# Optimization experiments

Hardware: AMD Instinct MI355X
Metric: run time of the kernel (lower is better)

## Reference

```python
import jax, jax.numpy as jnp
import numpy as np

N_NODES = 50000
N_EDGES = 800000
IN_C, HID_C, OUT_C = 128, 256, 64


def _linear_params(key, fan_in, fan_out):
    kw, kb = jax.random.split(key)
    bound = 1.0 / np.sqrt(fan_in)
    w = jax.random.uniform(kw, (fan_in, fan_out), jnp.float32, -bound, bound)
    b = jax.random.uniform(kb, (fan_out,), jnp.float32, -bound, bound)
    return w, b


def setup_inputs() -> dict:
    key = jax.random.key(0)
    ks = jax.random.split(key, 8)
    x = jax.random.normal(ks[0], (N_NODES, IN_C), jnp.float32)
    edge_index = jax.random.randint(ks[1], (2, N_EDGES), 0, N_NODES, dtype=jnp.int64)
    w1a, b1a = _linear_params(ks[2], IN_C, HID_C)
    w1b, b1b = _linear_params(ks[3], HID_C, HID_C)
    w2a, b2a = _linear_params(ks[4], HID_C, HID_C)
    w2b, b2b = _linear_params(ks[5], HID_C, HID_C)
    w3a, b3a = _linear_params(ks[6], HID_C, HID_C)
    w3b, b3b = _linear_params(ks[7], HID_C, OUT_C)
    return {
        "x": x, "edge_index": edge_index,
        "w1a": w1a, "b1a": b1a, "w1b": w1b, "b1b": b1b,
        "w2a": w2a, "b2a": b2a, "w2b": w2b, "b2b": b2b,
        "w3a": w3a, "b3a": b3a, "w3b": w3b, "b3b": b3b,
    }


def _gin_conv(x, src, dst, wa, ba, wb, bb):
    # GINConv (eps=0): MLP( x + sum_{j->i} x_j )
    agg = jax.ops.segment_sum(x[src], dst, num_segments=N_NODES)  # [N, d]
    h = x + agg
    h = jnp.maximum(h @ wa + ba, 0.0)
    return h @ wb + bb


def reference(x, edge_index, w1a, b1a, w1b, b1b, w2a, b2a, w2b, b2b,
              w3a, b3a, w3b, b3b):
    src, dst = edge_index[0], edge_index[1]
    h = jnp.maximum(_gin_conv(x, src, dst, w1a, b1a, w1b, b1b), 0.0)
    h = jnp.maximum(_gin_conv(h, src, dst, w2a, b2a, w2b, b2b), 0.0)
    # output head: Linear -> ReLU -> Dropout(eval: identity) -> Linear
    h = jnp.maximum(h @ w3a + b3a, 0.0)
    return h @ w3b + b3b  # [N, OUT_C]
```

## Files before the change

kernel.cpp:

```cpp
#include <hip/hip_runtime.h>
#include <stdint.h>

#define N_NODES 50000
#define N_EDGES 800000
#define M_PAD   50048
#define NREP    4
#define MCAP    8
#define SCAP    24
#define CSTR    50048
#define TSTR    264

typedef __attribute__((ext_vector_type(8))) short bf16x8;
typedef __attribute__((ext_vector_type(4))) float f32x4;

__device__ __forceinline__ unsigned short f2b(float f){
    unsigned int u = __builtin_bit_cast(unsigned int, f);
    u += 0x7fffu + ((u >> 16) & 1u);
    return (unsigned short)(u >> 16);
}
__device__ __forceinline__ float b2f(unsigned short s){
    unsigned int u = ((unsigned int)s) << 16;
    return __builtin_bit_cast(float, u);
}

__device__ __forceinline__ void gl_lds16(const void* g, void* l){
    __builtin_amdgcn_global_load_lds(
        (const __attribute__((address_space(1))) void*)g,
        (__attribute__((address_space(3))) void*)l, 16, 0, 0);
}

__global__ void k_x2b(const float* __restrict__ x, unsigned short* __restrict__ xs,
                      int* __restrict__ cnt){
    int gi = blockIdx.x * 256 + threadIdx.x;
    if (gi < NREP * CSTR) cnt[gi] = 0;
    size_t e0 = (size_t)gi * 8;
    if (e0 >= (size_t)M_PAD * 128) return;
    int node = (int)(e0 >> 7);
    int ch0  = (int)(e0 & 127);
    int sl = ch0 >> 5, wth = ch0 & 31;
    bf16x8 o;
    if (node < N_NODES){
        const float4* xp = (const float4*)(x + e0);
        float4 a = xp[0], b = xp[1];
        o[0] = (short)f2b(a.x); o[1] = (short)f2b(a.y);
        o[2] = (short)f2b(a.z); o[3] = (short)f2b(a.w);
        o[4] = (short)f2b(b.x); o[5] = (short)f2b(b.y);
        o[6] = (short)f2b(b.z); o[7] = (short)f2b(b.w);
    } else {
#pragma unroll
        for (int i = 0; i < 8; ++i) o[i] = 0;
    }
    *(bf16x8*)&xs[((size_t)(sl * 50048 + node)) * 32 + wth] = o;
}

__global__ void k_scatter(const int* __restrict__ ei, int* __restrict__ cnt,
                          unsigned short* __restrict__ mn, unsigned short* __restrict__ sp){
    int e = blockIdx.x * 256 + threadIdx.x;
    if (e < N_EDGES){
        unsigned d = (unsigned)ei[N_EDGES + e];
        unsigned s = (unsigned)ei[e];
        if (d < N_NODES && s < N_NODES){
            int r = threadIdx.x & 3;
            int p = atomicAdd(&cnt[r * CSTR + d], 1);
            int b = (d << 2) + r;
            if (p < MCAP) mn[(b << 3) + p] = (unsigned short)s;
            else if (p < MCAP + SCAP) sp[b * SCAP + (p - MCAP)] = (unsigned short)s;
        }
    }
}

template<int C, bool SPLIT>
__global__ __launch_bounds__(256) void k_aggx(const unsigned short* __restrict__ in,
        const int* __restrict__ cnt, const unsigned short* __restrict__ mn,
        const unsigned short* __restrict__ sp, unsigned short* __restrict__ out){
    constexpr int RS = C / 8;
    const int bid = blockIdx.x, w8 = bid & 7;
    int g, nbase;
    if (SPLIT){ g = w8 & 3; nbase = ((bid >> 3) + (w8 >> 2) * 1564) * 16; }
    else      { g = w8;     nbase = (bid >> 3) * 16; }
    const int lane = threadIdx.x & 63, wid = threadIdx.x >> 6;
    const int qd = lane >> 2, lq = lane & 3;
    const int nl = qd >> 2, r = qd & 3;
    const int n = nbase + wid * 4 + nl;
    const bf16x8* xr = (const bf16x8*)in;
    const size_t sb = (size_t)g * 50048;
    const int jz = N_NODES;

    float a[8];
#pragma unroll
    for (int i = 0; i < 8; ++i) a[i] = 0.f;

    int c = cnt[r * CSTR + n];
    int cr = (c > MCAP + SCAP) ? (MCAP + SCAP) : c;
    int c8 = (cr > MCAP) ? MCAP : cr;
    const unsigned short* mb = &mn[((n << 2) + r) << 3];
    ushort4 u0 = *(const ushort4*)mb;
    ushort4 u1 = *(const ushort4*)(mb + 4);

    {
        int j0 = (c8 > 0) ? (int)u0.x : jz;
        int j1 = (c8 > 1) ? (int)u0.y : jz;
        int j2 = (c8 > 2) ? (int)u0.z : jz;
        int j3 = (c8 > 3) ? (int)u0.w : jz;
        bf16x8 v0 = xr[(sb + j0) * 4 + lq];
        bf16x8 v1 = xr[(sb + j1) * 4 + lq];
        bf16x8 v2 = xr[(sb + j2) * 4 + lq];
        bf16x8 v3 = xr[(sb + j3) * 4 + lq];
#pragma unroll
        for (int i = 0; i < 8; ++i)
            a[i] += (b2f((unsigned short)v0[i]) + b2f((unsigned short)v1[i]))
                  + (b2f((unsigned short)v2[i]) + b2f((unsigned short)v3[i]));
    }
    if (c8 > 4){
        int j4 = (int)u1.x;
        int j5 = (c8 > 5) ? (int)u1.y : jz;
        int j6 = (c8 > 6) ? (int)u1.z : jz;
        int j7 = (c8 > 7) ? (int)u1.w : jz;
        bf16x8 v0 = xr[(sb + j4) * 4 + lq];
        bf16x8 v1 = xr[(sb + j5) * 4 + lq];
        bf16x8 v2 = xr[(sb + j6) * 4 + lq];
        bf16x8 v3 = xr[(sb + j7) * 4 + lq];
#pragma unroll
        for (int i = 0; i < 8; ++i)
            a[i] += (b2f((unsigned short)v0[i]) + b2f((unsigned short)v1[i]))
                  + (b2f((unsigned short)v2[i]) + b2f((unsigned short)v3[i]));
    }
    if (cr > MCAP){
        const unsigned short* sb2 = &sp[((n << 2) + r) * SCAP];
        for (int k = MCAP; k < cr; ++k){
            int j = sb2[k - MCAP];
            bf16x8 v = xr[(sb + j) * 4 + lq];
#pragma unroll
            for (int i = 0; i < 8; ++i) a[i] += b2f((unsigned short)v[i]);
        }
    }
#pragma unroll
    for (int i = 0; i < 8; ++i){
        a[i] += __shfl_xor(a[i], 4);
        a[i] += __shfl_xor(a[i], 8);
    }
    if (r == 0){
        bf16x8 o;
        if (n < N_NODES){
            bf16x8 s = xr[(sb + n) * 4 + lq];
#pragma unroll
            for (int i = 0; i < 8; ++i) o[i] = (short)f2b(a[i] + b2f((unsigned short)s[i]));
        } else {
#pragma unroll
            for (int i = 0; i < 8; ++i) o[i] = 0;
        }
        *(bf16x8*)&out[((size_t)n * RS + g * 4 + lq) * 8] = o;
    }
}

__global__ void k_wt_all(const float* w0, const float* w1, const float* w2,
                         const float* w3, const float* w4, const float* w5,
                         unsigned short* o0, unsigned short* o1, unsigned short* o2,
                         unsigned short* o3, unsigned short* o4, unsigned short* o5){
    const int Ks[6]  = {128, 256, 256, 256, 256, 256};
    const int Ns[6]  = {256, 256, 256, 256, 256,  64};
    const int NPs[6] = {256, 256, 256, 256, 256, 128};
    int s = blockIdx.y;
    const float* w = (s == 0) ? w0 : (s == 1) ? w1 : (s == 2) ? w2
                   : (s == 3) ? w3 : (s == 4) ? w4 : w5;
    unsigned short* o = (s == 0) ? o0 : (s == 1) ? o1 : (s == 2) ? o2
                      : (s == 3) ? o3 : (s == 4) ? o4 : o5;
    int K = Ks[s], N = Ns[s], NP = NPs[s];
    int idx = blockIdx.x * 256 + threadIdx.x;
    if (idx >= NP * K) return;
    int np = idx / K, k = idx - np * K;
    float v = (np < N) ? w[(size_t)k * N + np] : 0.f;
    o[idx] = f2b(v);
}

template<int K1, int NMID, int NOUT, bool RELU_OUT, bool BF16OUT, bool SLICED>
__global__ __launch_bounds__(256) void k_mlp2(const unsigned short* __restrict__ A,
        const unsigned short* __restrict__ WA, const float* __restrict__ bA,
        const unsigned short* __restrict__ WB, const float* __restrict__ bB,
        void* __restrict__ out, int mstore){
    constexpr int NFA = NMID / 32;
    constexpr int NFB = NOUT / 32;
    __shared__ alignas(16) unsigned short As[64 * 32];
    __shared__ alignas(16) unsigned short Bs[NMID * 32];
    __shared__ alignas(16) unsigned short T[64 * TSTR];
    const int tid  = threadIdx.x;
    const int lane = tid & 63;
    const int c = lane & 15, qq = lane >> 4;
    const int kk = qq * 8;
    const int row0 = blockIdx.x * 64;
    const int wm = (tid >> 6) >> 1, wn = (tid >> 6) & 1;

    const f32x4 fzero = {0.f, 0.f, 0.f, 0.f};
    const char* Ab = (const char*)A;

    {
        f32x4 acc[NFA][2];
#pragma unroll
        for (int nf = 0; nf < NFA; ++nf){ acc[nf][0] = fzero; acc[nf][1] = fzero; }
        const char* Wb = (const char*)WA;
        for (int kt = 0; kt < K1 / 32; ++kt){
            {
                const int o = tid * 16;
                gl_lds16(Ab + ((size_t)(row0 + (o >> 6)) * K1 + kt * 32) * 2 + (o & 63),
                         (char*)As + o);
            }
#pragma unroll
            for (int ch = 0; ch < NMID / 64; ++ch){
                const int o = ch * 4096 + tid * 16;
                gl_lds16(Wb + ((size_t)(o >> 6) * K1 + kt * 32) * 2 + (o & 63),
                         (char*)Bs + o);
            }
            __syncthreads();
            bf16x8 xf[2];
#pragma unroll
            for (int mf = 0; mf < 2; ++mf)
                xf[mf] = *(const bf16x8*)&As[(wm * 32 + mf * 16 + c) * 32 + kk];
#pragma unroll
            for (int nf = 0; nf < NFA; ++nf){
                bf16x8 wf = *(const bf16x8*)&Bs[((wn * NFA + nf) * 16 + c) * 32 + kk];
#pragma unroll
                for (int mf = 0; mf < 2; ++mf)
                    acc[nf][mf] = __builtin_amdgcn_mfma_f32_16x16x32_bf16(wf, xf[mf], acc[nf][mf], 0, 0, 0);
            }
            __syncthreads();
        }
#pragma unroll
        for (int nf = 0; nf < NFA; ++nf){
            const int nb = wn * (NFA * 16) + nf * 16 + qq * 4;
            const float4 bb = *(const float4*)&bA[nb];
#pragma unroll
            for (int mf = 0; mf < 2; ++mf){
                const int ml = wm * 32 + mf * 16 + c;
                float v0 = fmaxf(acc[nf][mf][0] + bb.x, 0.f);
                float v1 = fmaxf(acc[nf][mf][1] + bb.y, 0.f);
                float v2 = fmaxf(acc[nf][mf][2] + bb.z, 0.f);
                float v3 = fmaxf(acc[nf][mf][3] + bb.w, 0.f);
                uint2 p;
                p.x = (unsigned)f2b(v0) | ((unsigned)f2b(v1) << 16);
                p.y = (unsigned)f2b(v2) | ((unsigned)f2b(v3) << 16);
                *(uint2*)&T[ml * TSTR + nb] = p;
            }
        }
    }
    __syncthreads();

    {
        f32x4 acc[NFB][2];
#pragma unroll
        for (int nf = 0; nf < NFB; ++nf){ acc[nf][0] = fzero; acc[nf][1] = fzero; }
        const char* Wb = (const char*)WB;
        for (int kt = 0; kt < NMID / 32; ++kt){
#pragma unroll
            for (int ch = 0; ch < NOUT / 64; ++ch){
                const int o = ch * 4096 + tid * 16;
                gl_lds16(Wb + ((size_t)(o >> 6) * NMID + kt * 32) * 2 + (o & 63),
                         (char*)Bs + o);
            }
            __syncthreads();
            bf16x8 xf[2];
#pragma unroll
            for (int mf = 0; mf < 2; ++mf)
                xf[mf] = *(const bf16x8*)&T[(wm * 32 + mf * 16 + c) * TSTR + kt * 32 + kk];
#pragma unroll
            for (int nf = 0; nf < NFB; ++nf){
                bf16x8 wf = *(const bf16x8*)&Bs[((wn * NFB + nf) * 16 + c) * 32 + kk];
#pragma unroll
                for (int mf = 0; mf < 2; ++mf)
                    acc[nf][mf] = __builtin_amdgcn_mfma_f32_16x16x32_bf16(wf, xf[mf], acc[nf][mf], 0, 0, 0);
            }
            __syncthreads();
        }
#pragma unroll
        for (int nf = 0; nf < NFB; ++nf){
            const int nb = wn * (NFB * 16) + nf * 16 + qq * 4;
            const float4 bb = *(const float4*)&bB[nb];
#pragma unroll
            for (int mf = 0; mf < 2; ++mf){
                const int m = row0 + wm * 32 + mf * 16 + c;
                if (m < mstore){
                    float v0 = acc[nf][mf][0] + bb.x;
                    float v1 = acc[nf][mf][1] + bb.y;
                    float v2 = acc[nf][mf][2] + bb.z;
                    float v3 = acc[nf][mf][3] + bb.w;
                    if (RELU_OUT){
                        v0 = fmaxf(v0, 0.f); v1 = fmaxf(v1, 0.f);
                        v2 = fmaxf(v2, 0.f); v3 = fmaxf(v3, 0.f);
                    }
                    if (SLICED){
                        uint2 p;
                        p.x = (unsigned)f2b(v0) | ((unsigned)f2b(v1) << 16);
                        p.y = (unsigned)f2b(v2) | ((unsigned)f2b(v3) << 16);
                        if (m >= N_NODES){ p.x = 0; p.y = 0; }
                        *(uint2*)&((unsigned short*)out)[
                            ((size_t)((nb >> 5) * 50048 + m)) * 32 + (nb & 31)] = p;
                    } else if (BF16OUT){
                        uint2 p;
                        p.x = (unsigned)f2b(v0) | ((unsigned)f2b(v1) << 16);
                        p.y = (unsigned)f2b(v2) | ((unsigned)f2b(v3) << 16);
                        *(uint2*)&((unsigned short*)out)[(size_t)m * NOUT + nb] = p;
                    } else {
                        float4 p = make_float4(v0, v1, v2, v3);
                        *(float4*)&((float*)out)[(size_t)m * NOUT + nb] = p;
                    }
                }
            }
        }
    }
}

extern "C" void kernel_launch(void* const* d_in, const int* in_sizes, int n_in,
                              void* d_out, int out_size, void* d_ws, size_t ws_size,
                              hipStream_t stream){
    const float* x   = (const float*)d_in[0];
    const int*   ei  = (const int*)d_in[1];
    const float* w1a = (const float*)d_in[2];
    const float* b1a = (const float*)d_in[3];
    const float* w1b = (const float*)d_in[4];
    const float* b1b = (const float*)d_in[5];
    const float* w2a = (const float*)d_in[6];
    const float* b2a = (const float*)d_in[7];
    const float* w2b = (const float*)d_in[8];
    const float* b2b = (const float*)d_in[9];
    const float* w3a = (const float*)d_in[10];
    const float* b3a = (const float*)d_in[11];
    const float* w3b = (const float*)d_in[12];
    const float* b3b = (const float*)d_in[13];

    char* ws = (char*)d_ws;
    size_t off = 0;
    auto take = [&](size_t bytes) -> char* {
        off = (off + 255) & ~(size_t)255;
        char* p = ws + off;
        off += bytes;
        return p;
    };
    unsigned short* xs1  = (unsigned short*)take((size_t)4 * 50048 * 32 * 2);
    unsigned short* g1   = (unsigned short*)take((size_t)M_PAD * 128 * 2);
    unsigned short* h1s  = (unsigned short*)take((size_t)8 * 50048 * 32 * 2);
    unsigned short* g2   = (unsigned short*)take((size_t)M_PAD * 256 * 2);
    unsigned short* h2   = (unsigned short*)take((size_t)M_PAD * 256 * 2);
    unsigned short* wt1a = (unsigned short*)take(256 * 128 * 2);
    unsigned short* wt1b = (unsigned short*)take(256 * 256 * 2);
    unsigned short* wt2a = (unsigned short*)take(256 * 256 * 2);
    unsigned short* wt2b = (unsigned short*)take(256 * 256 * 2);
    unsigned short* wt3a = (unsigned short*)take(256 * 256 * 2);
    unsigned short* wt3b = (unsigned short*)take(128 * 256 * 2);
    int*            cnt  = (int*)take((size_t)NREP * CSTR * 4);
    unsigned short* mn   = (unsigned short*)take((size_t)M_PAD * 4 * MCAP * 2);
    unsigned short* sp   = (unsigned short*)take((size_t)M_PAD * 4 * SCAP * 2);

    k_x2b<<<(M_PAD * 128 / 8 + 255) / 256, 256, 0, stream>>>(x, xs1, cnt);
    k_scatter<<<(N_EDGES + 255) / 256, 256, 0, stream>>>(ei, cnt, mn, sp);
    k_wt_all<<<dim3(256, 6), 256, 0, stream>>>(w1a, w1b, w2a, w2b, w3a, w3b,
                                               wt1a, wt1b, wt2a, wt2b, wt3a, wt3b);

    k_aggx<128, true ><<<1564 * 8, 256, 0, stream>>>(xs1, cnt, mn, sp, g1);
    k_mlp2<128, 256, 256, true, true, true><<<M_PAD / 64, 256, 0, stream>>>(
        g1, wt1a, b1a, wt1b, b1b, h1s, M_PAD);
    k_aggx<256, false><<<3128 * 8, 256, 0, stream>>>(h1s, cnt, mn, sp, g2);
    k_mlp2<256, 256, 256, true, true, false><<<M_PAD / 64, 256, 0, stream>>>(
        g2, wt2a, b2a, wt2b, b2b, h2, M_PAD);
    k_mlp2<256, 256, 64, false, false, false><<<M_PAD / 64, 256, 0, stream>>>(
        h2, wt3a, b3a, wt3b, b3b, d_out, N_NODES);
}
```

Measured before the change: 235.2 us.

## Merge replicated neighbor buckets into per-node padded lists before aggregation

Adds a merge kernel that compacts the four replicated per-node neighbor buckets (main plus spill) into one contiguous list per node, padded to a multiple of four with a sentinel index. The aggregation kernel then assigns one quad of lanes per node instead of four quads, loops over groups of four gathers, and drops the cross-replica shuffle reduction and the conditional spill loop. This targets lane waste and divergence from uneven bucket fill, at the cost of an extra kernel and buffer. Lists are capped at 64 neighbors per node.

```diff
diff --git a/kernel.cpp b/kernel.cpp
--- a/kernel.cpp
+++ b/kernel.cpp
@@ -8,6 +8,7 @@
 #define MCAP    8
 #define SCAP    24
 #define CSTR    50048
+#define LCAP    64
 #define TSTR    264
 
 typedef __attribute__((ext_vector_type(8))) short bf16x8;
@@ -69,88 +70,80 @@
     }
 }
 
+__global__ void k_merge(const int* __restrict__ cnt, const unsigned short* __restrict__ mn,
+                        const unsigned short* __restrict__ sp,
+                        unsigned short* __restrict__ mg, int* __restrict__ gcnt){
+    const int t = threadIdx.x;
+    const int r = t & 3;
+    const int n = blockIdx.x * 64 + (t >> 2);
+    int c = cnt[r * CSTR + n];
+    if (c > MCAP + SCAP) c = MCAP + SCAP;
+    int incl = c;
+    int t1 = __shfl_up(incl, 1, 4); if (r >= 1) incl += t1;
+    int t2 = __shfl_up(incl, 2, 4); if (r >= 2) incl += t2;
+    const int excl = incl - c;
+    const int total = __shfl(incl, 3, 4);
+    const unsigned mb = (unsigned)n * LCAP;
+    const unsigned short* src = &mn[((n << 2) + r) << 3];
+    for (int i = 0; i < c && i < MCAP; ++i){
+        int pos = excl + i;
+        if (pos < LCAP) mg[mb + pos] = src[i];
+    }
+    const unsigned short* ssrc = &sp[((n << 2) + r) * SCAP];
+    for (int i = MCAP; i < c; ++i){
+        int pos = excl + i;
+        if (pos < LCAP) mg[mb + pos] = ssrc[i - MCAP];
+    }
+    if (r == 3){
+        int grp = (total + 3) >> 2;
+        if (grp > LCAP / 4) grp = LCAP / 4;
+        gcnt[n] = grp;
+        for (int pos = total; pos < grp * 4; ++pos) mg[mb + pos] = (unsigned short)N_NODES;
+    }
+}
+
 template<int C, bool SPLIT>
 __global__ __launch_bounds__(256) void k_aggx(const unsigned short* __restrict__ in,
-        const int* __restrict__ cnt, const unsigned short* __restrict__ mn,
-        const unsigned short* __restrict__ sp, unsigned short* __restrict__ out){
+        const int* __restrict__ gcnt, const unsigned short* __restrict__ mg,
+        unsigned short* __restrict__ out){
     constexpr int RS = C / 8;
     const int bid = blockIdx.x, w8 = bid & 7;
     int g, nbase;
-    if (SPLIT){ g = w8 & 3; nbase = ((bid >> 3) + (w8 >> 2) * 1564) * 16; }
-    else      { g = w8;     nbase = (bid >> 3) * 16; }
+    if (SPLIT){ g = w8 & 3; nbase = ((bid >> 3) + (w8 >> 2) * 391) * 64; }
+    else      { g = w8;     nbase = (bid >> 3) * 64; }
     const int lane = threadIdx.x & 63, wid = threadIdx.x >> 6;
     const int qd = lane >> 2, lq = lane & 3;
-    const int nl = qd >> 2, r = qd & 3;
-    const int n = nbase + wid * 4 + nl;
-    const bf16x8* xr = (const bf16x8*)in;
-    const size_t sb = (size_t)g * 50048;
-    const int jz = N_NODES;
+    const int n = nbase + wid * 16 + qd;
+    const bf16x8* __restrict__ xr = (const bf16x8*)in;
+    const unsigned sbu = (unsigned)g * 50048u;
 
     float a[8];
-#pragma unroll
-    for (int i = 0; i < 8; ++i) a[i] = 0.f;
-
-    int c = cnt[r * CSTR + n];
-    int cr = (c > MCAP + SCAP) ? (MCAP + SCAP) : c;
-    int c8 = (cr > MCAP) ? MCAP : cr;
-    const unsigned short* mb = &mn[((n << 2) + r) << 3];
-    ushort4 u0 = *(const ushort4*)mb;
-    ushort4 u1 = *(const ushort4*)(mb + 4);
-
     {
-        int j0 = (c8 > 0) ? (int)u0.x : jz;
-        int j1 = (c8 > 1) ? (int)u0.y : jz;
-        int j2 = (c8 > 2) ? (int)u0.z : jz;
-        int j3 = (c8 > 3) ? (int)u0.w : jz;
-        bf16x8 v0 = xr[(sb + j0) * 4 + lq];
-        bf16x8 v1 = xr[(sb + j1) * 4 + lq];
-        bf16x8 v2 = xr[(sb + j2) * 4 + lq];
-        bf16x8 v3 = xr[(sb + j3) * 4 + lq];
+        bf16x8 s = xr[(sbu + (unsigned)n) * 4u + (unsigned)lq];
+#pragma unroll
+        for (int i = 0; i < 8; ++i) a[i] = b2f((unsigned short)s[i]);
+    }
+    const int grp = gcnt[n];
+    const unsigned mbase = (unsigned)n * LCAP;
+    for (int k = 0; k < grp; ++k){
+        ushort4 jj = *(const ushort4*)&mg[mbase + (unsigned)(k * 4)];
+        unsigned i0 = (sbu + jj.x) * 4u + lq;
+        unsigned i1 = (sbu + jj.y) * 4u + lq;
+        unsigned i2 = (sbu + jj.z) * 4u + lq;
+        unsigned i3 = (sbu + jj.w) * 4u + lq;
+        bf16x8 v0 = xr[i0];
+        bf16x8 v1 = xr[i1];
+        bf16x8 v2 = xr[i2];
+        bf16x8 v3 = xr[i3];
 #pragma unroll
         for (int i = 0; i < 8; ++i)
             a[i] += (b2f((unsigned short)v0[i]) + b2f((unsigned short)v1[i]))
                   + (b2f((unsigned short)v2[i]) + b2f((unsigned short)v3[i]));
     }
-    if (c8 > 4){
-        int j4 = (int)u1.x;
-        int j5 = (c8 > 5) ? (int)u1.y : jz;
-        int j6 = (c8 > 6) ? (int)u1.z : jz;
-        int j7 = (c8 > 7) ? (int)u1.w : jz;
-        bf16x8 v0 = xr[(sb + j4) * 4 + lq];
-        bf16x8 v1 = xr[(sb + j5) * 4 + lq];
-        bf16x8 v2 = xr[(sb + j6) * 4 + lq];
-        bf16x8 v3 = xr[(sb + j7) * 4 + lq];
-#pragma unroll
-        for (int i = 0; i < 8; ++i)
-            a[i] += (b2f((unsigned short)v0[i]) + b2f((unsigned short)v1[i]))
-                  + (b2f((unsigned short)v2[i]) + b2f((unsigned short)v3[i]));
-    }
-    if (cr > MCAP){
-        const unsigned short* sb2 = &sp[((n << 2) + r) * SCAP];
-        for (int k = MCAP; k < cr; ++k){
-            int j = sb2[k - MCAP];
-            bf16x8 v = xr[(sb + j) * 4 + lq];
-#pragma unroll
-            for (int i = 0; i < 8; ++i) a[i] += b2f((unsigned short)v[i]);
-        }
-    }
-#pragma unroll
-    for (int i = 0; i < 8; ++i){
-        a[i] += __shfl_xor(a[i], 4);
-        a[i] += __shfl_xor(a[i], 8);
-    }
-    if (r == 0){
-        bf16x8 o;
-        if (n < N_NODES){
-            bf16x8 s = xr[(sb + n) * 4 + lq];
-#pragma unroll
-            for (int i = 0; i < 8; ++i) o[i] = (short)f2b(a[i] + b2f((unsigned short)s[i]));
-        } else {
-#pragma unroll
-            for (int i = 0; i < 8; ++i) o[i] = 0;
-        }
-        *(bf16x8*)&out[((size_t)n * RS + g * 4 + lq) * 8] = o;
-    }
+    bf16x8 o;
+#pragma unroll
+    for (int i = 0; i < 8; ++i) o[i] = (short)f2b(a[i]);
+    *(bf16x8*)&out[((unsigned)n * RS + (unsigned)(g * 4 + lq)) * 8u] = o;
 }
 
 __global__ void k_wt_all(const float* w0, const float* w1, const float* w2,
@@ -348,16 +341,19 @@
     int*            cnt  = (int*)take((size_t)NREP * CSTR * 4);
     unsigned short* mn   = (unsigned short*)take((size_t)M_PAD * 4 * MCAP * 2);
     unsigned short* sp   = (unsigned short*)take((size_t)M_PAD * 4 * SCAP * 2);
+    unsigned short* mg   = (unsigned short*)take((size_t)M_PAD * LCAP * 2);
+    int*            gcnt = (int*)take((size_t)M_PAD * 4);
 
     k_x2b<<<(M_PAD * 128 / 8 + 255) / 256, 256, 0, stream>>>(x, xs1, cnt);
     k_scatter<<<(N_EDGES + 255) / 256, 256, 0, stream>>>(ei, cnt, mn, sp);
+    k_merge<<<782, 256, 0, stream>>>(cnt, mn, sp, mg, gcnt);
     k_wt_all<<<dim3(256, 6), 256, 0, stream>>>(w1a, w1b, w2a, w2b, w3a, w3b,
                                                wt1a, wt1b, wt2a, wt2b, wt3a, wt3b);
 
-    k_aggx<128, true ><<<1564 * 8, 256, 0, stream>>>(xs1, cnt, mn, sp, g1);
+    k_aggx<128, true ><<<391 * 8, 256, 0, stream>>>(xs1, gcnt, mg, g1);
     k_mlp2<128, 256, 256, true, true, true><<<M_PAD / 64, 256, 0, stream>>>(
         g1, wt1a, b1a, wt1b, b1b, h1s, M_PAD);
-    k_aggx<256, false><<<3128 * 8, 256, 0, stream>>>(h1s, cnt, mn, sp, g2);
+    k_aggx<256, false><<<782 * 8, 256, 0, stream>>>(h1s, gcnt, mg, g2);
     k_mlp2<256, 256, 256, true, true, false><<<M_PAD / 64, 256, 0, stream>>>(
         g2, wt2a, b2a, wt2b, b2b, h2, M_PAD);
     k_mlp2<256, 256, 64, false, false, false><<<M_PAD / 64, 256, 0, stream>>>(
```

Result: slower. 240.6 us (+2.3%).
